# Kernel tuning notes

Measured on AMD Instinct MI355X. Metric: run time of the kernel, lower is better.

## Reference

```python
import jax, jax.numpy as jnp
import numpy as np
import math

# Model config (matches init_kwargs)
V, D, H, L, DFF, S_MAX = 32000, 512, 8, 6, 2048, 1024
DK = D // H


def _layernorm(x, g, b, eps=1e-5):
    m = jnp.mean(x, axis=-1, keepdims=True)
    v = jnp.mean(jnp.square(x - m), axis=-1, keepdims=True)
    return (x - m) / jnp.sqrt(v + eps) * g + b


def _pos_encoding(seq_len, d_model):
    # sin on even dims, cos on odd dims
    pos = jnp.arange(seq_len, dtype=jnp.float32)[:, None]          # [S,1]
    div = jnp.exp(jnp.arange(0, d_model, 2, dtype=jnp.float32) *
                  (-math.log(10000.0) / d_model))                   # [D/2]
    ang = pos * div                                                 # [S,D/2]
    pe = jnp.stack([jnp.sin(ang), jnp.cos(ang)], axis=-1)           # [S,D/2,2]
    return pe.reshape(seq_len, d_model)                             # [S,D]


def setup_inputs() -> dict:
    key = jax.random.key(0)
    ks = jax.random.split(key, 24)
    sd = 0.02

    def n(k, shape):
        return jax.random.normal(k, shape, jnp.float32) * sd

    B, S = 2, 1024
    return {
        "tokens": jax.random.randint(ks[0], (B, S), 0, V, dtype=jnp.int32),
        "tok_emb": n(ks[1], (V, D)),
        # attention projections, [L, D, D] stored as (in, out)
        "Wq": n(ks[2], (L, D, D)), "bq": jnp.zeros((L, D)),
        "Wk": n(ks[3], (L, D, D)), "bk": jnp.zeros((L, D)),
        "Wv": n(ks[4], (L, D, D)), "bv": jnp.zeros((L, D)),
        "Wo": n(ks[5], (L, D, D)), "bo": jnp.zeros((L, D)),
        "ln1_g": jnp.ones((L, D)), "ln1_b": jnp.zeros((L, D)),
        "W1": n(ks[6], (L, D, DFF)), "b1": jnp.zeros((L, DFF)),
        "W2": n(ks[7], (L, DFF, D)), "b2": jnp.zeros((L, D)),
        "ln2_g": jnp.ones((L, D)), "ln2_b": jnp.zeros((L, D)),
        "lnf_g": jnp.ones((D,)), "lnf_b": jnp.zeros((D,)),
        "Wout": n(ks[8], (D, V)), "bout": jnp.zeros((V,)),
    }


def reference(tokens, tok_emb, Wq, bq, Wk, bk, Wv, bv, Wo, bo,
              ln1_g, ln1_b, W1, b1, W2, b2, ln2_g, ln2_b,
              lnf_g, lnf_b, Wout, bout):
    B, S = tokens.shape
    x = tok_emb[tokens] * math.sqrt(D) + _pos_encoding(S, D)[None]   # [B,S,D]
    causal = jnp.tril(jnp.ones((S, S), dtype=bool))[None, None]       # [1,1,S,S]
    scale = math.sqrt(DK)

    attns = []
    for l in range(L):
        q = (x @ Wq[l] + bq[l]).reshape(B, S, H, DK).transpose(0, 2, 1, 3)
        k = (x @ Wk[l] + bk[l]).reshape(B, S, H, DK).transpose(0, 2, 1, 3)
        v = (x @ Wv[l] + bv[l]).reshape(B, S, H, DK).transpose(0, 2, 1, 3)
        scores = jnp.einsum('bhsk,bhtk->bhst', q, k) / scale           # [B,H,S,S]
        scores = jnp.where(causal, scores, -1e9)
        a = jax.nn.softmax(scores, axis=-1)
        ctx = jnp.einsum('bhst,bhtk->bhsk', a, v)                      # [B,H,S,DK]
        ctx = ctx.transpose(0, 2, 1, 3).reshape(B, S, D)
        attn_out = ctx @ Wo[l] + bo[l]
        x = _layernorm(x + attn_out, ln1_g[l], ln1_b[l])
        h = jax.nn.gelu(x @ W1[l] + b1[l], approximate=False)          # torch GELU (exact)
        ff = h @ W2[l] + b2[l]
        x = _layernorm(x + ff, ln2_g[l], ln2_b[l])
        attns.append(a)

    x = _layernorm(x, lnf_g, lnf_b)
    logits = x @ Wout + bout                                           # [B,S,V]
    return logits, jnp.stack(attns)                                    # attn: [L,B,H,S,S]
```

## Files before the change

### kernel.cpp

```cpp
#include <hip/hip_runtime.h>
#include <math.h>

#define NB 2
#define NS 1024
#define NH 8
#define NDK 64
#define ND 512
#define NDFF 2048
#define NV 32000
#define NL 6
#define MROWS (NB * NS)
#define QKVLD (3 * ND)

using bf16_t = __bf16;
using bf16x4 = __attribute__((ext_vector_type(4))) __bf16;
using bf16x8 = __attribute__((ext_vector_type(8))) __bf16;
using f32x4  = __attribute__((ext_vector_type(4))) float;

__device__ __forceinline__ void gload_lds16(const bf16_t* g, bf16_t* l) {
  __builtin_amdgcn_global_load_lds(
      (const __attribute__((address_space(1))) void*)g,
      (__attribute__((address_space(3))) void*)l, 16, 0, 0);
}

__device__ __forceinline__ float gelu_exact(float v) {
  return 0.5f * v * (1.0f + erff(v * 0.7071067811865476f));
}

__global__ __launch_bounds__(256)
void prep_kernel(const int* __restrict__ tokens, const float* __restrict__ emb,
                 const float* __restrict__ Wq, const float* __restrict__ Wk,
                 const float* __restrict__ Wv, const float* __restrict__ Wo,
                 const float* __restrict__ W1, const float* __restrict__ W2,
                 const float* __restrict__ Wout,
                 bf16_t* __restrict__ WqkvT, bf16_t* __restrict__ WoT,
                 bf16_t* __restrict__ W1T, bf16_t* __restrict__ W2T,
                 bf16_t* __restrict__ WoutT,
                 float* __restrict__ x, bf16_t* __restrict__ xb) {
  __shared__ bf16_t T[64][72];
  const int id = blockIdx.x;
  const int tid = threadIdx.x;

  if (id >= 8608) {
    const int row = id - 8608;
    const int s = row & (NS - 1);
    const int tok = tokens[row];
    const float SQRTD = 22.627416997969522f;
    const float C = -9.210340371976184f / (float)ND;
#pragma unroll
    for (int i = 0; i < 2; ++i) {
      const int d = tid + i * 256;
      const int pair = d >> 1;
      const float div = expf((float)(2 * pair) * C);
      const float ang = (float)s * div;
      const float pe = (d & 1) ? cosf(ang) : sinf(ang);
      const float v = emb[(size_t)tok * ND + d] * SQRTD + pe;
      x[(size_t)row * ND + d] = v;
      xb[(size_t)row * ND + d] = (bf16_t)v;
    }
    return;
  }

  const float* src; bf16_t* dst; int K, N, n0, k0;
  if (id < 1536) {
    const int z = id >> 6, t = id & 63;
    const int mat = z / 6, layer = z % 6;
    src = ((mat == 0) ? Wq : (mat == 1) ? Wk : (mat == 2) ? Wv : Wo) + (size_t)layer * ND * ND;
    dst = (mat < 3) ? (WqkvT + (size_t)layer * QKVLD * ND + (size_t)mat * ND * ND)
                    : (WoT + (size_t)layer * ND * ND);
    K = ND; N = ND; n0 = (t & 7) * 64; k0 = (t >> 3) * 64;
  } else if (id < 3072) {
    const int idx = id - 1536, layer = idx >> 8, t = idx & 255;
    src = W1 + (size_t)layer * ND * NDFF; dst = W1T + (size_t)layer * NDFF * ND;
    K = ND; N = NDFF; n0 = (t & 31) * 64; k0 = (t >> 5) * 64;
  } else if (id < 4608) {
    const int idx = id - 3072, layer = idx >> 8, t = idx & 255;
    src = W2 + (size_t)layer * NDFF * ND; dst = W2T + (size_t)layer * ND * NDFF;
    K = NDFF; N = ND; n0 = (t & 7) * 64; k0 = (t >> 3) * 64;
  } else {
    const int t = id - 4608;
    src = Wout; dst = WoutT;
    K = ND; N = NV; n0 = (t % 500) * 64; k0 = (t / 500) * 64;
  }

#pragma unroll
  for (int it = 0; it < 4; ++it) {
    const int k = (tid >> 4) + it * 16;
    const int c = (tid & 15) * 4;
    const float4 v = *(const float4*)&src[(size_t)(k0 + k) * N + n0 + c];
    T[c + 0][k] = (bf16_t)v.x;
    T[c + 1][k] = (bf16_t)v.y;
    T[c + 2][k] = (bf16_t)v.z;
    T[c + 3][k] = (bf16_t)v.w;
  }
  __syncthreads();
  const int n = tid >> 2, kk = (tid & 3) * 16;
  bf16x8 a = *(const bf16x8*)&T[n][kk];
  bf16x8 b2v = *(const bf16x8*)&T[n][kk + 8];
  *(bf16x8*)&dst[(size_t)(n0 + n) * K + k0 + kk] = a;
  *(bf16x8*)&dst[(size_t)(n0 + n) * K + k0 + kk + 8] = b2v;
}

__global__ __launch_bounds__(256)
void add_ln_kernel(float* __restrict__ x, const float* __restrict__ y0,
                   const float* __restrict__ y1,
                   const float* __restrict__ g, const float* __restrict__ bb,
                   const float* __restrict__ g2, const float* __restrict__ bb2,
                   bf16_t* __restrict__ xb) {
  const int row = blockIdx.x, tid = threadIdx.x;
  const size_t base = (size_t)row * ND;
  float v0 = x[base + tid], v1 = x[base + tid + 256];
  if (y0) { v0 += y0[base + tid]; v1 += y0[base + tid + 256]; }
  if (y1) { v0 += y1[base + tid]; v1 += y1[base + tid + 256]; }
  __shared__ float red[256];
  red[tid] = v0 + v1; __syncthreads();
  for (int o = 128; o > 0; o >>= 1) {
    if (tid < o) red[tid] += red[tid + o];
    __syncthreads();
  }
  const float mean = red[0] * (1.f / (float)ND);
  __syncthreads();
  const float d0 = v0 - mean, d1 = v1 - mean;
  red[tid] = d0 * d0 + d1 * d1; __syncthreads();
  for (int o = 128; o > 0; o >>= 1) {
    if (tid < o) red[tid] += red[tid + o];
    __syncthreads();
  }
  const float inv = 1.f / sqrtf(red[0] * (1.f / (float)ND) + 1e-5f);
  float o0 = d0 * inv * g[tid]       + bb[tid];
  float o1 = d1 * inv * g[tid + 256] + bb[tid + 256];

  if (g2) {
    __syncthreads();
    red[tid] = o0 + o1; __syncthreads();
    for (int o = 128; o > 0; o >>= 1) {
      if (tid < o) red[tid] += red[tid + o];
      __syncthreads();
    }
    const float mean2 = red[0] * (1.f / (float)ND);
    __syncthreads();
    const float e0 = o0 - mean2, e1 = o1 - mean2;
    red[tid] = e0 * e0 + e1 * e1; __syncthreads();
    for (int o = 128; o > 0; o >>= 1) {
      if (tid < o) red[tid] += red[tid + o];
      __syncthreads();
    }
    const float inv2 = 1.f / sqrtf(red[0] * (1.f / (float)ND) + 1e-5f);
    o0 = e0 * inv2 * g2[tid]       + bb2[tid];
    o1 = e1 * inv2 * g2[tid + 256] + bb2[tid + 256];
  } else {
    x[base + tid] = o0;
    x[base + tid + 256] = o1;
  }
  xb[base + tid] = (bf16_t)o0; xb[base + tid + 256] = (bf16_t)o1;
}

template <int ACT, int OUTBF>
__global__ __launch_bounds__(256)
void gemm_bt(const bf16_t* __restrict__ A, const bf16_t* __restrict__ Wt,
             const float* __restrict__ B0,
             void* __restrict__ Cout, int N, int K, int lda, int ldc) {
  __shared__ bf16_t As[128 * 64];
  __shared__ bf16_t Bs[128 * 64];
  const int tid = threadIdx.x, lane = tid & 63, w = tid >> 6;
  const int wm = w >> 1, wn = w & 1;
  const int lcol = lane & 15, hi = lane >> 4;

  const int nwg = gridDim.x * gridDim.y;
  const int flat = blockIdx.y * gridDim.x + blockIdx.x;
  const int q = nwg >> 3, r = nwg & 7;
  const int xcd = flat & 7, idx = flat >> 3;
  const int nf = (xcd < r ? xcd * (q + 1) : r * (q + 1) + (xcd - r) * q) + idx;
  const int m0 = (nf % gridDim.x) * 128, n0 = (nf / gridDim.x) * 128;

  const int sr8 = lane >> 3;
  const int sslot = lane & 7;

  f32x4 acc[4][4] = {};

  for (int k0 = 0; k0 < K; k0 += 64) {
#pragma unroll
    for (int t = 0; t < 2; ++t) {
#pragma unroll
      for (int c = 0; c < 2; ++c) {
        const int rbase = t * 64 + w * 16 + c * 8;
        const int row = rbase + sr8;
        const int ks = sslot ^ (row & 7);
        gload_lds16(&A[(size_t)(m0 + row) * lda + k0 + ks * 8], &As[rbase * 64]);
        gload_lds16(&Wt[(size_t)(n0 + row) * K + k0 + ks * 8], &Bs[rbase * 64]);
      }
    }
    __syncthreads();

#pragma unroll
    for (int kk = 0; kk < 2; ++kk) {
      bf16x8 af[4], bf[4];
#pragma unroll
      for (int m = 0; m < 4; ++m) {
        const int rr = wm * 64 + m * 16 + lcol;
        af[m] = *(const bf16x8*)&As[rr * 64 + (((kk * 4 + hi) ^ (rr & 7)) * 8)];
      }
#pragma unroll
      for (int n = 0; n < 4; ++n) {
        const int rr = wn * 64 + n * 16 + lcol;
        bf[n] = *(const bf16x8*)&Bs[rr * 64 + (((kk * 4 + hi) ^ (rr & 7)) * 8)];
      }
#pragma unroll
      for (int m = 0; m < 4; ++m)
#pragma unroll
        for (int n = 0; n < 4; ++n)
          acc[m][n] = __builtin_amdgcn_mfma_f32_16x16x32_bf16(bf[n], af[m], acc[m][n], 0, 0, 0);
    }
    __syncthreads();
  }

#pragma unroll
  for (int m = 0; m < 4; ++m) {
    const int row = m0 + wm * 64 + m * 16 + lcol;
#pragma unroll
    for (int n = 0; n < 4; ++n) {
      const int col = n0 + wn * 64 + n * 16 + hi * 4;
      const f32x4 bv = *(const f32x4*)&B0[col];
      f32x4 v;
#pragma unroll
      for (int i = 0; i < 4; ++i) {
        float t = acc[m][n][i] + bv[i];
        if (ACT == 1) t = gelu_exact(t);
        v[i] = t;
      }
      if (OUTBF) {
        bf16x4 o;
#pragma unroll
        for (int i = 0; i < 4; ++i) o[i] = (bf16_t)v[i];
        *(bf16x4*)&((bf16_t*)Cout)[(size_t)row * ldc + col] = o;
      } else {
        __builtin_nontemporal_store(v, (f32x4*)&((float*)Cout)[(size_t)row * ldc + col]);
      }
    }
  }
}

__global__ __launch_bounds__(256)
void gemm_qkv64(const bf16_t* __restrict__ A, const bf16_t* __restrict__ Wt,
                const float* __restrict__ B0, const float* __restrict__ B1,
                const float* __restrict__ B2,
                bf16_t* __restrict__ Cout, int K, int lda, int ldc) {
  __shared__ bf16_t As[64 * 128];
  __shared__ bf16_t Bs[64 * 128];
  const int tid = threadIdx.x, lane = tid & 63, w = tid >> 6;
  const int wm = w >> 1, wn = w & 1;
  const int lcol = lane & 15, hi = lane >> 4;
  const int m0 = blockIdx.x * 64, n0 = blockIdx.y * 64;
  const int sr4 = lane >> 4, sslot = lane & 15;

  f32x4 acc[2][2] = {};

  for (int k0 = 0; k0 < K; k0 += 128) {
#pragma unroll
    for (int c = 0; c < 4; ++c) {
      const int rbase = w * 16 + c * 4;
      const int row = rbase + sr4;
      const int ks = sslot ^ (row & 15);
      gload_lds16(&A[(size_t)(m0 + row) * lda + k0 + ks * 8], &As[rbase * 128]);
      gload_lds16(&Wt[(size_t)(n0 + row) * K + k0 + ks * 8], &Bs[rbase * 128]);
    }
    __syncthreads();

#pragma unroll
    for (int kk = 0; kk < 4; ++kk) {
      bf16x8 af[2], bf[2];
#pragma unroll
      for (int m = 0; m < 2; ++m) {
        const int rr = wm * 32 + m * 16 + lcol;
        af[m] = *(const bf16x8*)&As[rr * 128 + (((kk * 4 + hi) ^ (rr & 15)) * 8)];
      }
#pragma unroll
      for (int n = 0; n < 2; ++n) {
        const int rr = wn * 32 + n * 16 + lcol;
        bf[n] = *(const bf16x8*)&Bs[rr * 128 + (((kk * 4 + hi) ^ (rr & 15)) * 8)];
      }
#pragma unroll
      for (int m = 0; m < 2; ++m)
#pragma unroll
        for (int n = 0; n < 2; ++n)
          acc[m][n] = __builtin_amdgcn_mfma_f32_16x16x32_bf16(bf[n], af[m], acc[m][n], 0, 0, 0);
    }
    __syncthreads();
  }

#pragma unroll
  for (int m = 0; m < 2; ++m) {
    const int row = m0 + wm * 32 + m * 16 + lcol;
#pragma unroll
    for (int n = 0; n < 2; ++n) {
      const int col = n0 + wn * 32 + n * 16 + hi * 4;
      const int sel = col >> 9;
      const float* Bp = (sel == 0) ? B0 : (sel == 1) ? B1 : B2;
      const f32x4 bv = *(const f32x4*)&Bp[col & 511];
      bf16x4 o;
#pragma unroll
      for (int i = 0; i < 4; ++i) o[i] = (bf16_t)(acc[m][n][i] + bv[i]);
      *(bf16x4*)&Cout[(size_t)row * ldc + col] = o;
    }
  }
}

template <int ACT, int OUTBF>
__global__ __launch_bounds__(256)
void gemm64(const bf16_t* __restrict__ A, const bf16_t* __restrict__ Wt,
            const float* __restrict__ bias,
            void* __restrict__ Cout, int K, int lda, int ldc, size_t zstride) {
  __shared__ bf16_t As[64 * 128];
  __shared__ bf16_t Bs[64 * 128];
  const int tid = threadIdx.x, lane = tid & 63, w = tid >> 6;
  const int wm = w >> 1, wn = w & 1;
  const int lcol = lane & 15, hi = lane >> 4;
  const int m0 = blockIdx.x * 64, n0 = blockIdx.y * 64;
  const int sr4 = lane >> 4, sslot = lane & 15;
  const int kc = K / gridDim.z;
  const int kbeg = blockIdx.z * kc;

  f32x4 acc[2][2] = {};

  for (int k0 = kbeg; k0 < kbeg + kc; k0 += 128) {
#pragma unroll
    for (int c = 0; c < 4; ++c) {
      const int rbase = w * 16 + c * 4;
      const int row = rbase + sr4;
      const int ks = sslot ^ (row & 15);
      gload_lds16(&A[(size_t)(m0 + row) * lda + k0 + ks * 8], &As[rbase * 128]);
      gload_lds16(&Wt[(size_t)(n0 + row) * K + k0 + ks * 8], &Bs[rbase * 128]);
    }
    __syncthreads();

#pragma unroll
    for (int kk = 0; kk < 4; ++kk) {
      bf16x8 af[2], bf[2];
#pragma unroll
      for (int m = 0; m < 2; ++m) {
        const int rr = wm * 32 + m * 16 + lcol;
        af[m] = *(const bf16x8*)&As[rr * 128 + (((kk * 4 + hi) ^ (rr & 15)) * 8)];
      }
#pragma unroll
      for (int n = 0; n < 2; ++n) {
        const int rr = wn * 32 + n * 16 + lcol;
        bf[n] = *(const bf16x8*)&Bs[rr * 128 + (((kk * 4 + hi) ^ (rr & 15)) * 8)];
      }
#pragma unroll
      for (int m = 0; m < 2; ++m)
#pragma unroll
        for (int n = 0; n < 2; ++n)
          acc[m][n] = __builtin_amdgcn_mfma_f32_16x16x32_bf16(bf[n], af[m], acc[m][n], 0, 0, 0);
    }
    __syncthreads();
  }

#pragma unroll
  for (int m = 0; m < 2; ++m) {
    const int row = m0 + wm * 32 + m * 16 + lcol;
#pragma unroll
    for (int n = 0; n < 2; ++n) {
      const int col = n0 + wn * 32 + n * 16 + hi * 4;
      f32x4 bv = {0.f, 0.f, 0.f, 0.f};
      if (blockIdx.z == 0) bv = *(const f32x4*)&bias[col];
      f32x4 v;
#pragma unroll
      for (int i = 0; i < 4; ++i) {
        float t = acc[m][n][i] + bv[i];
        if (ACT == 1) t = gelu_exact(t);
        v[i] = t;
      }
      if (OUTBF) {
        bf16x4 o;
#pragma unroll
        for (int i = 0; i < 4; ++i) o[i] = (bf16_t)v[i];
        *(bf16x4*)&((bf16_t*)Cout)[(size_t)row * ldc + col] = o;
      } else {
        *(f32x4*)&((float*)Cout)[blockIdx.z * zstride + (size_t)row * ldc + col] = v;
      }
    }
  }
}

__global__ __launch_bounds__(256)
void attn_fused(const bf16_t* __restrict__ qkv, float* __restrict__ probs,
                bf16_t* __restrict__ ctx) {
  const int p = blockIdx.x;
  const int h = blockIdx.y, b = blockIdx.z;
  const int q0A = p * 32;
  const int q0B = NS - 32 - q0A;
  const int qmaxA = q0A + 31, qmaxB = q0B + 31;
  const int NTT = (qmaxB >> 7) + 1;
  const int tid = threadIdx.x, lane = tid & 63, wq = tid >> 6;
  const int lcol = lane & 15, hi = lane >> 4;

  __shared__ bf16_t Qs[64][72];
  __shared__ bf16_t Ks[128][72];
  __shared__ bf16_t Vs[64][132];
  __shared__ bf16_t Ps[64][132];

  const int qrow  = (wq < 2) ? (q0A + wq * 16 + lcol) : (q0B + (wq - 2) * 16 + lcol);
  const int qmaxW = (wq < 2) ? qmaxA : qmaxB;

  {
    const int z0 = NTT * 128;
    const int nz = (NS - z0) >> 2;
    if (nz > 0) {
      const f32x4 zf = {0.f, 0.f, 0.f, 0.f};
      for (int idx = tid; idx < 64 * nz; idx += 256) {
        const int r = idx / nz, c = (idx - r * nz) * 4;
        const int grow = (r < 32) ? (q0A + r) : (q0B + r - 32);
        __builtin_nontemporal_store(zf,
            (f32x4*)&probs[(((size_t)b * NH + h) * NS + grow) * NS + z0 + c]);
      }
    }
  }

  {
    const int r = tid >> 2, c = (tid & 3) * 16;
    const int grow = (r < 32) ? (q0A + r) : (q0B + r - 32);
    const bf16_t* src = &qkv[((size_t)(b * NS + grow)) * QKVLD + h * NDK + c];
    *(bf16x8*)&Qs[r][c]     = *(const bf16x8*)&src[0];
    *(bf16x8*)&Qs[r][c + 8] = *(const bf16x8*)&src[8];
  }
  __syncthreads();
  const bf16x8 qf0 = *(const bf16x8*)&Qs[wq * 16 + lcol][hi * 8];
  const bf16x8 qf1 = *(const bf16x8*)&Qs[wq * 16 + lcol][32 + hi * 8];
  const float scale = 0.125f;

  float m_run = -1e30f, s_run = 0.f;

  for (int tt = 0; tt < NTT; ++tt) {
    const int t0 = tt * 128;
    const int fmax = min(8, ((qmaxW - t0) >> 4) + 1);
    {
      const int r = tid >> 1, cb = (tid & 1) * 32;
      const bf16_t* src = &qkv[((size_t)(b * NS + t0 + r)) * QKVLD + ND + h * NDK + cb];
#pragma unroll
      for (int j = 0; j < 4; ++j)
        *(bf16x8*)&Ks[r][cb + j * 8] = *(const bf16x8*)&src[j * 8];
    }
    __syncthreads();

    float tmax = -1e30f;
    f32x4 sc[8];
#pragma unroll
    for (int f = 0; f < 8; ++f) {
      if (f >= fmax) break;
      f32x4 s4 = {};
      const bf16x8 ka0 = *(const bf16x8*)&Ks[f * 16 + lcol][hi * 8];
      const bf16x8 ka1 = *(const bf16x8*)&Ks[f * 16 + lcol][32 + hi * 8];
      s4 = __builtin_amdgcn_mfma_f32_16x16x32_bf16(ka0, qf0, s4, 0, 0, 0);
      s4 = __builtin_amdgcn_mfma_f32_16x16x32_bf16(ka1, qf1, s4, 0, 0, 0);
#pragma unroll
      for (int i = 0; i < 4; ++i) {
        const int t = t0 + f * 16 + hi * 4 + i;
        const float v = (t <= qrow) ? s4[i] * scale : -1e30f;
        s4[i] = v;
        tmax = fmaxf(tmax, v);
      }
      sc[f] = s4;
    }
    tmax = fmaxf(tmax, __shfl_xor(tmax, 16));
    tmax = fmaxf(tmax, __shfl_xor(tmax, 32));
    const float m_new = fmaxf(m_run, tmax);
    float sum = 0.f;
#pragma unroll
    for (int f = 0; f < 8; ++f) {
      if (f >= fmax) break;
#pragma unroll
      for (int i = 0; i < 4; ++i) sum += __expf(sc[f][i] - m_new);
    }
    sum += __shfl_xor(sum, 16);
    sum += __shfl_xor(sum, 32);
    s_run = s_run * __expf(m_run - m_new) + sum;
    m_run = m_new;
    __syncthreads();
  }
  const float inv = 1.f / s_run;

  f32x4 cacc[4] = {};
  const size_t prow = (((size_t)b * NH + h) * NS + qrow) * NS;
  for (int tt = NTT - 1; tt >= 0; --tt) {
    const int t0 = tt * 128;
    const int fmax = min(8, ((qmaxW - t0) >> 4) + 1);
    if (tt != NTT - 1) {
      const int r = tid >> 1, cb = (tid & 1) * 32;
      const bf16_t* src = &qkv[((size_t)(b * NS + t0 + r)) * QKVLD + ND + h * NDK + cb];
#pragma unroll
      for (int j = 0; j < 4; ++j)
        *(bf16x8*)&Ks[r][cb + j * 8] = *(const bf16x8*)&src[j * 8];
    }
    {
#pragma unroll
      for (int it = 0; it < 2; ++it) {
        const int t4 = (tid >> 4) * 4 + it * 64;
        const int dk4 = (tid & 15) * 4;
        bf16x4 rr[4];
#pragma unroll
        for (int i = 0; i < 4; ++i)
          rr[i] = *(const bf16x4*)&qkv[((size_t)(b * NS + t0 + t4 + i)) * QKVLD + 2 * ND + h * NDK + dk4];
#pragma unroll
        for (int j = 0; j < 4; ++j) {
          bf16x4 c;
#pragma unroll
          for (int i = 0; i < 4; ++i) c[i] = rr[i][j];
          *(bf16x4*)&Vs[dk4 + j][t4] = c;
        }
      }
    }
    __syncthreads();

    const f32x4 zf = {0.f, 0.f, 0.f, 0.f};
    const bf16x4 zb = {(bf16_t)0.f, (bf16_t)0.f, (bf16_t)0.f, (bf16_t)0.f};
#pragma unroll
    for (int f = 0; f < 8; ++f) {
      if (f < fmax) {
        f32x4 s4 = {};
        const bf16x8 ka0 = *(const bf16x8*)&Ks[f * 16 + lcol][hi * 8];
        const bf16x8 ka1 = *(const bf16x8*)&Ks[f * 16 + lcol][32 + hi * 8];
        s4 = __builtin_amdgcn_mfma_f32_16x16x32_bf16(ka0, qf0, s4, 0, 0, 0);
        s4 = __builtin_amdgcn_mfma_f32_16x16x32_bf16(ka1, qf1, s4, 0, 0, 0);
        f32x4 pw;
        bf16x4 pb;
#pragma unroll
        for (int i = 0; i < 4; ++i) {
          const int t = t0 + f * 16 + hi * 4 + i;
          const float v = (t <= qrow) ? s4[i] * scale : -1e30f;
          const float pr = __expf(v - m_run) * inv;
          pw[i] = pr;
          pb[i] = (bf16_t)pr;
        }
        __builtin_nontemporal_store(pw, (f32x4*)&probs[prow + t0 + f * 16 + hi * 4]);
        *(bf16x4*)&Ps[wq * 16 + lcol][f * 16 + hi * 4] = pb;
      } else {
        __builtin_nontemporal_store(zf, (f32x4*)&probs[prow + t0 + f * 16 + hi * 4]);
        *(bf16x4*)&Ps[wq * 16 + lcol][f * 16 + hi * 4] = zb;
      }
    }

    if (fmax > 0) {
#pragma unroll
      for (int ks = 0; ks < 4; ++ks) {
        const bf16x8 pf = *(const bf16x8*)&Ps[wq * 16 + lcol][ks * 32 + hi * 8];
#pragma unroll
        for (int df = 0; df < 4; ++df) {
          const bf16x8 vf = *(const bf16x8*)&Vs[df * 16 + lcol][ks * 32 + hi * 8];
          cacc[df] = __builtin_amdgcn_mfma_f32_16x16x32_bf16(vf, pf, cacc[df], 0, 0, 0);
        }
      }
    }
    __syncthreads();
  }

#pragma unroll
  for (int df = 0; df < 4; ++df) {
    bf16x4 o;
#pragma unroll
    for (int i = 0; i < 4; ++i) o[i] = (bf16_t)cacc[df][i];
    *(bf16x4*)&ctx[((size_t)(b * NS + qrow)) * ND + h * NDK + df * 16 + hi * 4] = o;
  }
}

extern "C" void kernel_launch(void* const* d_in, const int* in_sizes, int n_in,
                              void* d_out, int out_size, void* d_ws, size_t ws_size,
                              hipStream_t stream) {
  const int*   tokens  = (const int*)d_in[0];
  const float* tok_emb = (const float*)d_in[1];
  const float* Wq = (const float*)d_in[2];
  const float* bq = (const float*)d_in[3];
  const float* Wk = (const float*)d_in[4];
  const float* bk = (const float*)d_in[5];
  const float* Wv = (const float*)d_in[6];
  const float* bv = (const float*)d_in[7];
  const float* Wo = (const float*)d_in[8];
  const float* bo = (const float*)d_in[9];
  const float* ln1_g = (const float*)d_in[10];
  const float* ln1_b = (const float*)d_in[11];
  const float* W1 = (const float*)d_in[12];
  const float* b1 = (const float*)d_in[13];
  const float* W2 = (const float*)d_in[14];
  const float* b2 = (const float*)d_in[15];
  const float* ln2_g = (const float*)d_in[16];
  const float* ln2_b = (const float*)d_in[17];
  const float* lnf_g = (const float*)d_in[18];
  const float* lnf_b = (const float*)d_in[19];
  const float* Wout = (const float*)d_in[20];
  const float* bout = (const float*)d_in[21];

  float* logits   = (float*)d_out;
  float* attn_all = (float*)d_out + (size_t)NB * NS * NV;

  char* w = (char*)d_ws;
  float* x    = (float*)w;  w += (size_t)4 << 20;
  float* tmp  = (float*)w;  w += (size_t)8 << 20;
  bf16_t* xb  = (bf16_t*)w; w += (size_t)2 << 20;
  bf16_t* qkv = (bf16_t*)w; w += (size_t)6 << 20;
  bf16_t* ctx = (bf16_t*)w; w += (size_t)2 << 20;
  bf16_t* hh  = (bf16_t*)w; w += (size_t)8 << 20;
  bf16_t* WqkvT = (bf16_t*)w; w += (size_t)6 * QKVLD * ND * 2;
  bf16_t* WoT   = (bf16_t*)w; w += (size_t)6 * ND * ND * 2;
  bf16_t* W1T   = (bf16_t*)w; w += (size_t)6 * NDFF * ND * 2;
  bf16_t* W2T   = (bf16_t*)w; w += (size_t)6 * ND * NDFF * 2;
  bf16_t* WoutT = (bf16_t*)w; w += (size_t)NV * ND * 2;
  if ((size_t)(w - (char*)d_ws) > ws_size) return;

  const int M = MROWS;
  const size_t U = (size_t)M * ND;
  float* tmp1 = tmp + U;

  prep_kernel<<<10656, 256, 0, stream>>>(tokens, tok_emb, Wq, Wk, Wv, Wo, W1, W2, Wout,
                                         WqkvT, WoT, W1T, W2T, WoutT, x, xb);

  const dim3 gQKV(M / 64, QKVLD / 64);
  const dim3 gFF1(M / 64, NDFF / 64);
  const dim3 gOut(M / 128, NV / 128);
  const dim3 g64s(M / 64, ND / 64, 2);
  const dim3 gAttn(16, NH, NB);

  for (int l = 0; l < NL; ++l) {
    gemm_qkv64<<<gQKV, 256, 0, stream>>>(xb, WqkvT + (size_t)l * QKVLD * ND,
        bq + l * ND, bk + l * ND, bv + l * ND, qkv, ND, ND, QKVLD);

    float* probs_l = attn_all + (size_t)l * NB * NH * NS * NS;
    attn_fused<<<gAttn, 256, 0, stream>>>(qkv, probs_l, ctx);

    gemm64<0, 0><<<g64s, 256, 0, stream>>>(ctx, WoT + (size_t)l * ND * ND,
        bo + l * ND, tmp, ND, ND, ND, U);
    add_ln_kernel<<<M, 256, 0, stream>>>(x, tmp, tmp1,
        ln1_g + l * ND, ln1_b + l * ND, nullptr, nullptr, xb);

    gemm64<1, 1><<<gFF1, 256, 0, stream>>>(xb, W1T + (size_t)l * NDFF * ND,
        b1 + l * NDFF, hh, ND, ND, NDFF, 0);
    gemm64<0, 0><<<g64s, 256, 0, stream>>>(hh, W2T + (size_t)l * ND * NDFF,
        b2 + l * ND, tmp, NDFF, NDFF, ND, U);
    add_ln_kernel<<<M, 256, 0, stream>>>(x, tmp, tmp1,
        ln2_g + l * ND, ln2_b + l * ND,
        (l == NL - 1) ? lnf_g : nullptr, (l == NL - 1) ? lnf_b : nullptr, xb);
  }

  gemm_bt<0, 0><<<gOut, 256, 0, stream>>>(xb, WoutT, bout,
      logits, NV, ND, ND, NV);
}
```

Before: 692.6 us.

## Split attention into stats and PV kernels with key-tile halves and concatenated-ctx reduction

Replaces the fused attention kernel with two kernels. The first computes per-row softmax max and sum over interleaved key tiles, split across two halves. The second combines the two halves' statistics, writes probabilities and a partial PV result per half into a concatenated context buffer. The Wo GEMM then sums the two halves by treating them as K=1024, masking the weight's K index so both halves reuse the same weights. This doubles the grid to improve parallelism and load balance. The cost is an extra launch, a round trip of the statistics through global memory, and a larger context buffer that aliases the FFN hidden buffer.

```diff
diff --git a/kernel.cpp b/kernel.cpp
--- a/kernel.cpp
+++ b/kernel.cpp
@@ -309,7 +309,8 @@
 __global__ __launch_bounds__(256)
 void gemm64(const bf16_t* __restrict__ A, const bf16_t* __restrict__ Wt,
             const float* __restrict__ bias,
-            void* __restrict__ Cout, int K, int lda, int ldc, size_t zstride) {
+            void* __restrict__ Cout, int K, int lda, int ldw, int kmask,
+            int ldc, size_t zstride) {
   __shared__ bf16_t As[64 * 128];
   __shared__ bf16_t Bs[64 * 128];
   const int tid = threadIdx.x, lane = tid & 63, w = tid >> 6;
@@ -329,7 +330,7 @@
       const int row = rbase + sr4;
       const int ks = sslot ^ (row & 15);
       gload_lds16(&A[(size_t)(m0 + row) * lda + k0 + ks * 8], &As[rbase * 128]);
-      gload_lds16(&Wt[(size_t)(n0 + row) * K + k0 + ks * 8], &Bs[rbase * 128]);
+      gload_lds16(&Wt[(size_t)(n0 + row) * ldw + ((k0 & kmask) + ks * 8)], &Bs[rbase * 128]);
     }
     __syncthreads();
 
@@ -383,56 +384,37 @@
 }
 
 __global__ __launch_bounds__(256)
-void attn_fused(const bf16_t* __restrict__ qkv, float* __restrict__ probs,
-                bf16_t* __restrict__ ctx) {
-  const int p = blockIdx.x;
-  const int h = blockIdx.y, b = blockIdx.z;
-  const int q0A = p * 32;
-  const int q0B = NS - 32 - q0A;
-  const int qmaxA = q0A + 31, qmaxB = q0B + 31;
-  const int NTT = (qmaxB >> 7) + 1;
+void attn_stats(const bf16_t* __restrict__ qkv,
+                float* __restrict__ marr, float* __restrict__ sarr) {
+  const int qt = 15 - blockIdx.x;
+  const int h = blockIdx.y;
+  const int b = blockIdx.z >> 1, half = blockIdx.z & 1;
+  const int q0 = qt * 64;
+  const int NTT = (q0 >> 7) + 1;
+  const int qmax = q0 + 63;
   const int tid = threadIdx.x, lane = tid & 63, wq = tid >> 6;
   const int lcol = lane & 15, hi = lane >> 4;
 
   __shared__ bf16_t Qs[64][72];
   __shared__ bf16_t Ks[128][72];
-  __shared__ bf16_t Vs[64][132];
-  __shared__ bf16_t Ps[64][132];
-
-  const int qrow  = (wq < 2) ? (q0A + wq * 16 + lcol) : (q0B + (wq - 2) * 16 + lcol);
-  const int qmaxW = (wq < 2) ? qmaxA : qmaxB;
-
-  {
-    const int z0 = NTT * 128;
-    const int nz = (NS - z0) >> 2;
-    if (nz > 0) {
-      const f32x4 zf = {0.f, 0.f, 0.f, 0.f};
-      for (int idx = tid; idx < 64 * nz; idx += 256) {
-        const int r = idx / nz, c = (idx - r * nz) * 4;
-        const int grow = (r < 32) ? (q0A + r) : (q0B + r - 32);
-        __builtin_nontemporal_store(zf,
-            (f32x4*)&probs[(((size_t)b * NH + h) * NS + grow) * NS + z0 + c]);
-      }
-    }
-  }
 
   {
     const int r = tid >> 2, c = (tid & 3) * 16;
-    const int grow = (r < 32) ? (q0A + r) : (q0B + r - 32);
-    const bf16_t* src = &qkv[((size_t)(b * NS + grow)) * QKVLD + h * NDK + c];
+    const bf16_t* src = &qkv[((size_t)(b * NS + q0 + r)) * QKVLD + h * NDK + c];
     *(bf16x8*)&Qs[r][c]     = *(const bf16x8*)&src[0];
     *(bf16x8*)&Qs[r][c + 8] = *(const bf16x8*)&src[8];
   }
   __syncthreads();
   const bf16x8 qf0 = *(const bf16x8*)&Qs[wq * 16 + lcol][hi * 8];
   const bf16x8 qf1 = *(const bf16x8*)&Qs[wq * 16 + lcol][32 + hi * 8];
+  const int qrow = q0 + wq * 16 + lcol;
   const float scale = 0.125f;
 
   float m_run = -1e30f, s_run = 0.f;
 
-  for (int tt = 0; tt < NTT; ++tt) {
+  for (int tt = half; tt < NTT; tt += 2) {
     const int t0 = tt * 128;
-    const int fmax = min(8, ((qmaxW - t0) >> 4) + 1);
+    const int fmax = min(8, ((qmax - t0) >> 4) + 1);
     {
       const int r = tid >> 1, cb = (tid & 1) * 32;
       const bf16_t* src = &qkv[((size_t)(b * NS + t0 + r)) * QKVLD + ND + h * NDK + cb];
@@ -477,14 +459,71 @@
     m_run = m_new;
     __syncthreads();
   }
-  const float inv = 1.f / s_run;
+
+  if (hi == 0) {
+    const size_t idx = (((size_t)half * NB + b) * NH + h) * NS + qrow;
+    marr[idx] = m_run;
+    sarr[idx] = s_run;
+  }
+}
+
+__global__ __launch_bounds__(256)
+void attn_pv(const bf16_t* __restrict__ qkv,
+             const float* __restrict__ marr, const float* __restrict__ sarr,
+             float* __restrict__ probs, bf16_t* __restrict__ ctxcat) {
+  const int qt = 15 - blockIdx.x;
+  const int h = blockIdx.y;
+  const int b = blockIdx.z >> 1, half = blockIdx.z & 1;
+  const int q0 = qt * 64;
+  const int NTT = (q0 >> 7) + 1;
+  const int qmax = q0 + 63;
+  const int tid = threadIdx.x, lane = tid & 63, wq = tid >> 6;
+  const int lcol = lane & 15, hi = lane >> 4;
+
+  __shared__ bf16_t Qs[64][72];
+  __shared__ bf16_t Ks[128][72];
+  __shared__ bf16_t Vs[64][132];
+  __shared__ bf16_t Ps[64][132];
+
+  if (half == 0) {
+    const int z0 = NTT * 128;
+    const int nz = (NS - z0) >> 2;
+    if (nz > 0) {
+      const f32x4 zf = {0.f, 0.f, 0.f, 0.f};
+      for (int idx = tid; idx < 64 * nz; idx += 256) {
+        const int r = idx / nz, c = (idx - r * nz) * 4;
+        __builtin_nontemporal_store(zf,
+            (f32x4*)&probs[(((size_t)b * NH + h) * NS + q0 + r) * NS + z0 + c]);
+      }
+    }
+  }
+
+  {
+    const int r = tid >> 2, c = (tid & 3) * 16;
+    const bf16_t* src = &qkv[((size_t)(b * NS + q0 + r)) * QKVLD + h * NDK + c];
+    *(bf16x8*)&Qs[r][c]     = *(const bf16x8*)&src[0];
+    *(bf16x8*)&Qs[r][c + 8] = *(const bf16x8*)&src[8];
+  }
+  __syncthreads();
+  const bf16x8 qf0 = *(const bf16x8*)&Qs[wq * 16 + lcol][hi * 8];
+  const bf16x8 qf1 = *(const bf16x8*)&Qs[wq * 16 + lcol][32 + hi * 8];
+  const int qrow = q0 + wq * 16 + lcol;
+  const float scale = 0.125f;
+
+  const size_t i0 = (((size_t)0 * NB + b) * NH + h) * NS + qrow;
+  const size_t i1 = (((size_t)1 * NB + b) * NH + h) * NS + qrow;
+  const float m0 = marr[i0], m1 = marr[i1];
+  const float s0 = sarr[i0], s1 = sarr[i1];
+  const float m_fin = fmaxf(m0, m1);
+  const float s_fin = s0 * __expf(m0 - m_fin) + s1 * __expf(m1 - m_fin);
+  const float inv = 1.f / s_fin;
 
   f32x4 cacc[4] = {};
   const size_t prow = (((size_t)b * NH + h) * NS + qrow) * NS;
-  for (int tt = NTT - 1; tt >= 0; --tt) {
+  for (int tt = half; tt < NTT; tt += 2) {
     const int t0 = tt * 128;
-    const int fmax = min(8, ((qmaxW - t0) >> 4) + 1);
-    if (tt != NTT - 1) {
+    const int fmax = min(8, ((qmax - t0) >> 4) + 1);
+    {
       const int r = tid >> 1, cb = (tid & 1) * 32;
       const bf16_t* src = &qkv[((size_t)(b * NS + t0 + r)) * QKVLD + ND + h * NDK + cb];
 #pragma unroll
@@ -527,7 +566,7 @@
         for (int i = 0; i < 4; ++i) {
           const int t = t0 + f * 16 + hi * 4 + i;
           const float v = (t <= qrow) ? s4[i] * scale : -1e30f;
-          const float pr = __expf(v - m_run) * inv;
+          const float pr = __expf(v - m_fin) * inv;
           pw[i] = pr;
           pb[i] = (bf16_t)pr;
         }
@@ -539,15 +578,13 @@
       }
     }
 
-    if (fmax > 0) {
-#pragma unroll
-      for (int ks = 0; ks < 4; ++ks) {
-        const bf16x8 pf = *(const bf16x8*)&Ps[wq * 16 + lcol][ks * 32 + hi * 8];
-#pragma unroll
-        for (int df = 0; df < 4; ++df) {
-          const bf16x8 vf = *(const bf16x8*)&Vs[df * 16 + lcol][ks * 32 + hi * 8];
-          cacc[df] = __builtin_amdgcn_mfma_f32_16x16x32_bf16(vf, pf, cacc[df], 0, 0, 0);
-        }
+#pragma unroll
+    for (int ks = 0; ks < 4; ++ks) {
+      const bf16x8 pf = *(const bf16x8*)&Ps[wq * 16 + lcol][ks * 32 + hi * 8];
+#pragma unroll
+      for (int df = 0; df < 4; ++df) {
+        const bf16x8 vf = *(const bf16x8*)&Vs[df * 16 + lcol][ks * 32 + hi * 8];
+        cacc[df] = __builtin_amdgcn_mfma_f32_16x16x32_bf16(vf, pf, cacc[df], 0, 0, 0);
       }
     }
     __syncthreads();
@@ -558,7 +595,7 @@
     bf16x4 o;
 #pragma unroll
     for (int i = 0; i < 4; ++i) o[i] = (bf16_t)cacc[df][i];
-    *(bf16x4*)&ctx[((size_t)(b * NS + qrow)) * ND + h * NDK + df * 16 + hi * 4] = o;
+    *(bf16x4*)&ctxcat[((size_t)(b * NS + qrow)) * 1024 + half * 512 + h * NDK + df * 16 + hi * 4] = o;
   }
 }
 
@@ -596,8 +633,12 @@
   float* tmp  = (float*)w;  w += (size_t)8 << 20;
   bf16_t* xb  = (bf16_t*)w; w += (size_t)2 << 20;
   bf16_t* qkv = (bf16_t*)w; w += (size_t)6 << 20;
-  bf16_t* ctx = (bf16_t*)w; w += (size_t)2 << 20;
-  bf16_t* hh  = (bf16_t*)w; w += (size_t)8 << 20;
+  float* marr = (float*)w;
+  float* sarr = (float*)(w + (512 << 10));
+  w += (size_t)2 << 20;
+  bf16_t* hh  = (bf16_t*)w;
+  bf16_t* ctxcat = (bf16_t*)w;
+  w += (size_t)8 << 20;
   bf16_t* WqkvT = (bf16_t*)w; w += (size_t)6 * QKVLD * ND * 2;
   bf16_t* WoT   = (bf16_t*)w; w += (size_t)6 * ND * ND * 2;
   bf16_t* W1T   = (bf16_t*)w; w += (size_t)6 * NDFF * ND * 2;
@@ -616,24 +657,27 @@
   const dim3 gFF1(M / 64, NDFF / 64);
   const dim3 gOut(M / 128, NV / 128);
   const dim3 g64s(M / 64, ND / 64, 2);
-  const dim3 gAttn(16, NH, NB);
+  const dim3 gAttn(16, NH, NB * 2);
+
+  const int ALLK = 0x7fffffff;
 
   for (int l = 0; l < NL; ++l) {
     gemm_qkv64<<<gQKV, 256, 0, stream>>>(xb, WqkvT + (size_t)l * QKVLD * ND,
         bq + l * ND, bk + l * ND, bv + l * ND, qkv, ND, ND, QKVLD);
 
     float* probs_l = attn_all + (size_t)l * NB * NH * NS * NS;
-    attn_fused<<<gAttn, 256, 0, stream>>>(qkv, probs_l, ctx);
-
-    gemm64<0, 0><<<g64s, 256, 0, stream>>>(ctx, WoT + (size_t)l * ND * ND,
-        bo + l * ND, tmp, ND, ND, ND, U);
+    attn_stats<<<gAttn, 256, 0, stream>>>(qkv, marr, sarr);
+    attn_pv<<<gAttn, 256, 0, stream>>>(qkv, marr, sarr, probs_l, ctxcat);
+
+    gemm64<0, 0><<<g64s, 256, 0, stream>>>(ctxcat, WoT + (size_t)l * ND * ND,
+        bo + l * ND, tmp, 1024, 1024, ND, 511, ND, U);
     add_ln_kernel<<<M, 256, 0, stream>>>(x, tmp, tmp1,
         ln1_g + l * ND, ln1_b + l * ND, nullptr, nullptr, xb);
 
     gemm64<1, 1><<<gFF1, 256, 0, stream>>>(xb, W1T + (size_t)l * NDFF * ND,
-        b1 + l * NDFF, hh, ND, ND, NDFF, 0);
+        b1 + l * NDFF, hh, ND, ND, ND, ALLK, NDFF, 0);
     gemm64<0, 0><<<g64s, 256, 0, stream>>>(hh, W2T + (size_t)l * ND * NDFF,
-        b2 + l * ND, tmp, NDFF, NDFF, ND, U);
+        b2 + l * ND, tmp, NDFF, NDFF, NDFF, ALLK, ND, U);
     add_ln_kernel<<<M, 256, 0, stream>>>(x, tmp, tmp1,
         ln2_g + l * ND, ln2_b + l * ND,
         (l == NL - 1) ? lnf_g : nullptr, (l == NL - 1) ? lnf_b : nullptr, xb);
```

New measurement: 649.4 us. -6.2%, faster.
